# Performance work log

Hardware: AMD Instinct MI355X
Metric: run time of the kernel (lower is better)

Reference implementation:

```python
import jax, jax.numpy as jnp
import numpy as np

B, P, T, V, E, D, ENC = 64, 196, 64, 10000, 512, 512, 512


def setup_inputs() -> dict:
    key = jax.random.key(0)
    ks = jax.random.split(key, 12)
    encoder_out = jax.random.normal(ks[0], (B, P, ENC), jnp.float32)
    encoder_captions = jax.random.randint(ks[1], (B, T), 0, V)
    lens = jax.random.randint(ks[2], (B,), 2, T + 1)
    caption_len = jnp.sort(lens)[::-1].at[0].set(T)  # descending, max pinned to T
    g = lambda k, shape: jax.random.normal(k, shape, jnp.float32) * 0.02
    embedding = jax.random.uniform(ks[3], (V, E), jnp.float32, -0.1, 0.1)
    W_ih = g(ks[4], (4 * D, E + ENC)); b_ih = jnp.zeros((4 * D,), jnp.float32)
    W_hh = g(ks[5], (4 * D, D)); b_hh = jnp.zeros((4 * D,), jnp.float32)
    W_h0 = g(ks[6], (D, ENC)); b_h0 = jnp.zeros((D,), jnp.float32)
    W_c0 = g(ks[7], (D, ENC)); b_c0 = jnp.zeros((D,), jnp.float32)
    W_fc = jax.random.uniform(ks[8], (V, D), jnp.float32, -0.1, 0.1)
    b_fc = jnp.zeros((V,), jnp.float32)
    return dict(encoder_out=encoder_out, encoder_captions=encoder_captions,
                caption_len=caption_len, embedding=embedding,
                W_ih=W_ih, b_ih=b_ih, W_hh=W_hh, b_hh=b_hh,
                W_h0=W_h0, b_h0=b_h0, W_c0=W_c0, b_c0=b_c0,
                W_fc=W_fc, b_fc=b_fc)


def reference(encoder_out, encoder_captions, caption_len, embedding,
              W_ih, b_ih, W_hh, b_hh, W_h0, b_h0, W_c0, b_c0, W_fc, b_fc):
    Tdec = encoder_captions.shape[1] - 1  # max(decode_lengths) since max len pinned
    emb = embedding[encoder_captions]  # [B, T, E]
    mean_enc = encoder_out.mean(axis=1)  # [B, ENC]
    sum_enc = encoder_out.sum(axis=1)    # [B, ENC] (constant across timesteps)
    h0 = mean_enc @ W_h0.T + b_h0
    c0 = mean_enc @ W_c0.T + b_c0
    dec_len = caption_len - 1

    def step(carry, xs):
        h, c = carry
        emb_t, active = xs  # emb_t: [B, E], active: [B] bool
        x = jnp.concatenate([emb_t, sum_enc], axis=1)  # [B, E+ENC]
        gates = x @ W_ih.T + b_ih + h @ W_hh.T + b_hh  # [B, 4D]
        i, f, g, o = jnp.split(gates, 4, axis=1)
        i = jax.nn.sigmoid(i); f = jax.nn.sigmoid(f)
        o = jax.nn.sigmoid(o); g = jnp.tanh(g)
        c_new = f * c + i * g
        h_new = o * jnp.tanh(c_new)
        m = active[:, None]
        # rows past their decode length keep frozen state; preds zero there
        h2 = jnp.where(m, h_new, h)
        c2 = jnp.where(m, c_new, c)
        preds = jnp.where(m, h_new @ W_fc.T + b_fc, 0.0)  # dropout = identity (eval)
        return (h2, c2), preds

    emb_seq = jnp.swapaxes(emb[:, :Tdec], 0, 1)  # [Tdec, B, E]
    active = jnp.arange(Tdec)[:, None] < dec_len[None, :]  # [Tdec, B]
    _, preds = jax.lax.scan(step, (h0, c0), (emb_seq, active))
    return jnp.swapaxes(preds, 0, 1)  # [B, Tdec, V]
```

## Files before the change

kernel.cpp:

```cpp
#include <hip/hip_runtime.h>

typedef __attribute__((ext_vector_type(8))) short bf16x8;
typedef __attribute__((ext_vector_type(4))) float f32x4;
typedef __attribute__((ext_vector_type(2))) float f32x2;
typedef __attribute__((ext_vector_type(4))) unsigned int u32x4;

__device__ __forceinline__ unsigned short f2bf(float x) {
  union { float f; unsigned u; } v; v.f = x;
  unsigned r = v.u + 0x7fffu + ((v.u >> 16) & 1u);
  return (unsigned short)(r >> 16);
}
__device__ __forceinline__ float bf2f(unsigned short s) {
  union { unsigned u; float f; } v; v.u = ((unsigned)s) << 16;
  return v.f;
}
__device__ __forceinline__ float sigm(float x) { return 1.f / (1.f + __expf(-x)); }
__device__ __forceinline__ float tanh_fast(float x) { return 2.f * sigm(2.f * x) - 1.f; }

typedef const __attribute__((address_space(1))) void gvoid_t;
typedef __attribute__((address_space(3))) void lvoid_t;
__device__ __forceinline__ void gl16(const void* g, void* l) {
  __builtin_amdgcn_global_load_lds((gvoid_t*)g, (lvoid_t*)l, 16, 0, 0);
}

__device__ __forceinline__ void ldh16_sc1(const unsigned short* p, u32x4 o[16]) {
  asm volatile(
      "global_load_dwordx4 %0, %16, off sc1\n\t"
      "global_load_dwordx4 %1, %16, off offset:64 sc1\n\t"
      "global_load_dwordx4 %2, %16, off offset:128 sc1\n\t"
      "global_load_dwordx4 %3, %16, off offset:192 sc1\n\t"
      "global_load_dwordx4 %4, %16, off offset:256 sc1\n\t"
      "global_load_dwordx4 %5, %16, off offset:320 sc1\n\t"
      "global_load_dwordx4 %6, %16, off offset:384 sc1\n\t"
      "global_load_dwordx4 %7, %16, off offset:448 sc1\n\t"
      "global_load_dwordx4 %8, %16, off offset:512 sc1\n\t"
      "global_load_dwordx4 %9, %16, off offset:576 sc1\n\t"
      "global_load_dwordx4 %10, %16, off offset:640 sc1\n\t"
      "global_load_dwordx4 %11, %16, off offset:704 sc1\n\t"
      "global_load_dwordx4 %12, %16, off offset:768 sc1\n\t"
      "global_load_dwordx4 %13, %16, off offset:832 sc1\n\t"
      "global_load_dwordx4 %14, %16, off offset:896 sc1\n\t"
      "global_load_dwordx4 %15, %16, off offset:960 sc1\n\t"
      "s_waitcnt vmcnt(0)"
      : "=&v"(o[0]), "=&v"(o[1]), "=&v"(o[2]), "=&v"(o[3]), "=&v"(o[4]),
        "=&v"(o[5]), "=&v"(o[6]), "=&v"(o[7]), "=&v"(o[8]), "=&v"(o[9]),
        "=&v"(o[10]), "=&v"(o[11]), "=&v"(o[12]), "=&v"(o[13]), "=&v"(o[14]),
        "=&v"(o[15])
      : "v"(p)
      : "memory");
}
__device__ __forceinline__ void st2_sc1(unsigned* p, unsigned v0, unsigned v1) {
  asm volatile("global_store_dword %0, %1, off sc1\n\t"
               "global_store_dword %0, %2, off offset:1024 sc1" ::"v"(p), "v"(v0),
               "v"(v1) : "memory");
}
__device__ __forceinline__ void ldpgt_sc1(const unsigned short* p0,
                                          const unsigned short* p1,
                                          const unsigned short* p2,
                                          const unsigned short* p3, unsigned o[4]) {
  asm volatile(
      "global_load_dword %0, %4, off sc1\n\t"
      "global_load_dword %1, %5, off sc1\n\t"
      "global_load_dword %2, %6, off sc1\n\t"
      "global_load_dword %3, %7, off sc1\n\t"
      "s_waitcnt vmcnt(0)"
      : "=&v"(o[0]), "=&v"(o[1]), "=&v"(o[2]), "=&v"(o[3])
      : "v"(p0), "v"(p1), "v"(p2), "v"(p3)
      : "memory");
}
__device__ __forceinline__ void sts_sc1(unsigned short* p, unsigned short v) {
  asm volatile("global_store_short %0, %1, off sc1" ::"v"(p), "v"((unsigned)v)
               : "memory");
}

#define B_ 64
#define TDEC 63
#define D_ 512
#define V_ 10000
#define NWG 32
#define NCONS 223
#define NTILE_N 79
#define NTILE_M 32

__global__ __launch_bounds__(256) void prep(
    const float* __restrict__ enc,
    const float* __restrict__ Wh0, const float* __restrict__ Wc0,
    const float* __restrict__ Wih, const float* __restrict__ Whh,
    const float* __restrict__ Wfc, const float* __restrict__ emb,
    const int* __restrict__ caps,
    short* __restrict__ Wcat, short* __restrict__ Wihe, short* __restrict__ Whhb,
    short* __restrict__ Wfcb, short* __restrict__ Xemb,
    unsigned short* __restrict__ Hall, unsigned short* __restrict__ App) {
  if (blockIdx.x < 128) {
    int b = blockIdx.x >> 1;
    int d = (blockIdx.x & 1) * 256 + threadIdx.x;
    const float* p = enc + (long)b * 196 * 512 + d;
    float s = 0.f;
#pragma unroll 4
    for (int i = 0; i < 196; ++i) s += p[(long)i * 512];
    unsigned short hi = f2bf(s);
    unsigned short lo = f2bf(s - bf2f(hi));
    App[b * 1536 + d] = hi;
    App[b * 1536 + 512 + d] = hi;
    App[b * 1536 + 1024 + d] = lo;
  }
  const long N1 = 3072L * 1536;
  const long N2 = N1 + 2048L * 512;
  const long N3 = N2 + 2048L * 512;
  const long N4 = N3 + 10112L * 512;
  const long N5 = N4 + 4096L * 512;
  const long N6 = N5 + 64L * 512;
  const long N7 = N6 + 64L * 1536;
  for (long idx = (long)blockIdx.x * 256 + threadIdx.x; idx < N7; idx += 2048L * 256) {
    if (idx < N1) {
      int j = (int)(idx / 1536);
      int kk = (int)(idx - (long)j * 1536);
      int k = kk & 511, seg = kk >> 9;
      const float* src = (j < 512) ? (Wh0 + (long)j * 512)
                       : (j < 1024) ? (Wc0 + (long)(j - 512) * 512)
                                    : (Wih + (long)(j - 1024) * 1024 + 512);
      float x = src[k];
      unsigned short hi = f2bf(x);
      Wcat[idx] = (seg == 1) ? (short)f2bf(x - bf2f(hi)) : (short)hi;
    } else if (idx < N2) {
      long e = idx - N1;
      Wihe[e] = (short)f2bf(Wih[(e >> 9) * 1024 + (e & 511)]);
    } else if (idx < N3) {
      long e = idx - N2;
      Whhb[e] = (short)f2bf(Whh[e]);
    } else if (idx < N4) {
      long e = idx - N3;
      long j = e >> 9;
      Wfcb[e] = (j < V_) ? (short)f2bf(Wfc[e]) : (short)0;
    } else if (idx < N5) {
      long e = idx - N4;
      int m = (int)(e >> 9), k = (int)(e & 511);
      short v = 0;
      if (m < B_ * TDEC) {
        int t = m >> 6, b = m & 63;
        int tok = caps[b * 64 + t];
        v = (short)f2bf(emb[(long)tok * 512 + k]);
      }
      Xemb[e] = v;
    } else if (idx < N6) {
      long e = idx - N5;
      Hall[(long)B_ * TDEC * 512 + e] = 0;
    } else {
      long e = idx - N6;
      App[64L * 1536 + e] = 0;
    }
  }
}

__global__ __launch_bounds__(256) void gemm128(
    const short* __restrict__ A, const short* __restrict__ Bm, int K,
    float* __restrict__ f0, float* __restrict__ f1, float* __restrict__ f2,
    unsigned short* __restrict__ sb,
    const float* __restrict__ b0, const float* __restrict__ b1,
    const float* __restrict__ b2, const float* __restrict__ b3) {
  __shared__ short Al[4096], Bl[4096];
  const int tid = threadIdx.x, lane = tid & 63, w = tid >> 6;
  const int wr = w >> 1, wc = w & 1;
  const long m0 = 0, n0 = (long)blockIdx.x * 128;
  f32x4 zz = {0.f, 0.f, 0.f, 0.f};
  f32x4 acc[4][4];
#pragma unroll
  for (int i = 0; i < 4; ++i)
#pragma unroll
    for (int j = 0; j < 4; ++j) acc[i][j] = zz;

  const int srow = tid >> 2, scol = (tid & 3) * 8;
  const short* Ag = A + (m0 + srow) * K + scol;
  const short* Bg = Bm + (n0 + srow) * K + scol;
  short* Alw = &Al[w * 512];
  short* Blw = &Bl[w * 512];
  const int la = (lane & 15) * 32 + (lane >> 4) * 8;

  for (int k0 = 0; k0 < K; k0 += 32) {
    __syncthreads();
    gl16(Ag + k0, Alw);
    gl16(Ag + (long)64 * K + k0, Alw + 2048);
    gl16(Bg + k0, Blw);
    gl16(Bg + (long)64 * K + k0, Blw + 2048);
    __syncthreads();
    bf16x8 af[4], bfr[4];
#pragma unroll
    for (int mi = 0; mi < 4; ++mi) af[mi] = *(const bf16x8*)&Al[(wr * 64 + mi * 16) * 32 + la];
#pragma unroll
    for (int ni = 0; ni < 4; ++ni) bfr[ni] = *(const bf16x8*)&Bl[(wc * 64 + ni * 16) * 32 + la];
#pragma unroll
    for (int mi = 0; mi < 4; ++mi)
#pragma unroll
      for (int ni = 0; ni < 4; ++ni)
        acc[mi][ni] = __builtin_amdgcn_mfma_f32_16x16x32_bf16(af[mi], bfr[ni], acc[mi][ni], 0, 0, 0);
  }

  if (wr == 1) return;
#pragma unroll
  for (int mi = 0; mi < 4; ++mi) {
#pragma unroll
    for (int ni = 0; ni < 4; ++ni) {
      int n = (int)n0 + wc * 64 + ni * 16 + (lane & 15);
#pragma unroll
      for (int reg = 0; reg < 4; ++reg) {
        int m = mi * 16 + (lane >> 4) * 4 + reg;
        float v = acc[mi][ni][reg];
        if (n < 512) {
          float r = v * (1.f / 196.f) + b0[n];
          f0[m * 512 + n] = r;
          sb[m * 512 + n] = f2bf(r);
        } else if (n < 1024) {
          int nn = n - 512;
          float r = v * (1.f / 196.f) + b1[nn];
          f1[m * 512 + nn] = r;
        } else {
          int nn = n - 1024;
          f2[(long)nn * 64 + m] = v + b2[nn] + b3[nn];
        }
      }
    }
  }
}

__global__ __launch_bounds__(512, 1) void lstm_fused(
    const short* __restrict__ Whhb, const float* __restrict__ ENCCT,
    unsigned short* __restrict__ PGT, const float* __restrict__ h0f,
    const float* __restrict__ c0f, const int* __restrict__ caplen,
    unsigned short* __restrict__ hbuf, unsigned short* __restrict__ Hall,
    const short* __restrict__ Wfcb, const float* __restrict__ bfc,
    float* __restrict__ out, int* __restrict__ flags,
    const short* __restrict__ Xemb, const short* __restrict__ Wihe) {
  __shared__ short SH[64 * 512];
  const int bid = blockIdx.x;
  const int tid = threadIdx.x, lane = tid & 63, w = tid >> 6;
  int* prog = flags + 2048;
  int* mcnt = flags + 2304;

  if (bid == NWG) {
    if (w != 0) return;
    int cur = 0;
    while (cur < TDEC) {
      int v = TDEC;
      if (lane < NWG)
        v = __hip_atomic_load(&flags[lane * 32], __ATOMIC_RELAXED,
                              __HIP_MEMORY_SCOPE_AGENT);
      int m = v;
#pragma unroll
      for (int o = 32; o; o >>= 1) {
        int t2 = __shfl_xor(m, o, 64);
        m = (t2 < m) ? t2 : m;
      }
      if (lane == 0 && m > cur)
        __hip_atomic_store(prog, m, __ATOMIC_RELAXED, __HIP_MEMORY_SCOPE_AGENT);
      cur = m;
    }
    return;
  }

  if (bid < NWG) {
    short* Wl = SH;
    const int wg = bid, d0 = wg * 16;
    const int br = w >> 1, rc = w & 1;

    for (int it = tid; it < 4096; it += 512) {
      int r = it >> 6, c8 = it & 63;
      int g = (r >> 3) & 3, rcc = r >> 5, dl_ = r & 7;
      int j = g * 512 + d0 + rcc * 8 + dl_;
      bf16x8 v = *(const bf16x8*)(Whhb + (long)j * 512 + c8 * 8);
      *(bf16x8*)&Wl[r * 512 + ((c8 * 8) ^ ((r & 7) << 3))] = v;
    }

    const int q = (lane >> 4) & 3, bit3 = (lane >> 3) & 1, dl = lane & 7;
    const int d = d0 + rc * 8 + dl;
    const int b0 = br * 16 + q * 4 + 2 * bit3;
    const int ji = d, jf = 512 + d, jg = 1024 + d, jo = 1536 + d;

    f32x2 ei = *(const f32x2*)(ENCCT + (long)ji * 64 + b0);
    f32x2 ef = *(const f32x2*)(ENCCT + (long)jf * 64 + b0);
    f32x2 eg = *(const f32x2*)(ENCCT + (long)jg * 64 + b0);
    f32x2 eo = *(const f32x2*)(ENCCT + (long)jo * 64 + b0);
    float c_r[2] = {c0f[b0 * 512 + d], c0f[(b0 + 1) * 512 + d]};
    float h_r[2] = {h0f[b0 * 512 + d], h0f[(b0 + 1) * 512 + d]};
    int dlen0 = caplen[b0] - 1, dlen1 = caplen[b0 + 1] - 1;
    __syncthreads();

    const int arow = br * 16 + (lane & 15);
    const int kgo = (lane >> 4) * 8;
    const int r0 = rc * 32 + (lane & 15), r1 = rc * 32 + 16 + (lane & 15);
    const int sw0 = (r0 & 7) << 3, sw1 = (r1 & 7) << 3;

    int lastmt = -1;
    unsigned pgw[4];
#define WAIT_MT(mt_)                                                          \
    {                                                                         \
      int ok;                                                                 \
      do {                                                                    \
        int c = 0;                                                            \
        if (lane == 0)                                                        \
          c = __hip_atomic_load(&mcnt[(mt_) * 32], __ATOMIC_RELAXED,          \
                                __HIP_MEMORY_SCOPE_AGENT);                    \
        ok = __shfl(c, 0, 64);                                                \
      } while (ok < 16);                                                      \
    }
    WAIT_MT(0);
    lastmt = 0;
    ldpgt_sc1(PGT + (long)ji * 64 + b0, PGT + (long)jf * 64 + b0,
              PGT + (long)jg * 64 + b0, PGT + (long)jo * 64 + b0, pgw);

    for (int t = 0; t < TDEC; ++t) {
      const unsigned short* hsrc = hbuf + (t & 1) * 32768;
      union { u32x4 u[16]; bf16x8 v[16]; } av;
      ldh16_sc1(hsrc + arow * 512 + kgo, av.u);
      f32x4 a0A = {0.f, 0.f, 0.f, 0.f}, a0B = a0A, a1A = a0A, a1B = a0A;
#pragma unroll
      for (int kk = 0; kk < 8; ++kk) {
        int kA = kk * 32 + kgo, kB = (kk + 8) * 32 + kgo;
        a0A = __builtin_amdgcn_mfma_f32_16x16x32_bf16(
            av.v[kk], *(const bf16x8*)&Wl[r0 * 512 + (kA ^ sw0)], a0A, 0, 0, 0);
        a1A = __builtin_amdgcn_mfma_f32_16x16x32_bf16(
            av.v[kk], *(const bf16x8*)&Wl[r1 * 512 + (kA ^ sw1)], a1A, 0, 0, 0);
        a0B = __builtin_amdgcn_mfma_f32_16x16x32_bf16(
            av.v[kk + 8], *(const bf16x8*)&Wl[r0 * 512 + (kB ^ sw0)], a0B, 0, 0, 0);
        a1B = __builtin_amdgcn_mfma_f32_16x16x32_bf16(
            av.v[kk + 8], *(const bf16x8*)&Wl[r1 * 512 + (kB ^ sw1)], a1B, 0, 0, 0);
      }
      f32x4 a0 = a0A + a0B, a1 = a1A + a1B;

      float own00 = bit3 ? a0[2] : a0[0], own01 = bit3 ? a0[3] : a0[1];
      float snd00 = bit3 ? a0[0] : a0[2], snd01 = bit3 ? a0[1] : a0[3];
      float own10 = bit3 ? a1[2] : a1[0], own11 = bit3 ? a1[3] : a1[1];
      float snd10 = bit3 ? a1[0] : a1[2], snd11 = bit3 ? a1[1] : a1[3];
      float rcv00 = __shfl_xor(snd00, 8, 64), rcv01 = __shfl_xor(snd01, 8, 64);
      float rcv10 = __shfl_xor(snd10, 8, 64), rcv11 = __shfl_xor(snd11, 8, 64);
      float iv[2], fv[2], gv[2], ov[2];
      iv[0] = bit3 ? rcv00 : own00; iv[1] = bit3 ? rcv01 : own01;
      fv[0] = bit3 ? own00 : rcv00; fv[1] = bit3 ? own01 : rcv01;
      gv[0] = bit3 ? rcv10 : own10; gv[1] = bit3 ? rcv11 : own11;
      ov[0] = bit3 ? own10 : rcv10; ov[1] = bit3 ? own11 : rcv11;

      unsigned short hall0, hall1, hs0, hs1;
#pragma unroll
      for (int r = 0; r < 2; ++r) {
        float ii = iv[r] + ei[r] + bf2f((unsigned short)(r ? (pgw[0] >> 16) : (pgw[0] & 0xffffu)));
        float ff = fv[r] + ef[r] + bf2f((unsigned short)(r ? (pgw[1] >> 16) : (pgw[1] & 0xffffu)));
        float gg = gv[r] + eg[r] + bf2f((unsigned short)(r ? (pgw[2] >> 16) : (pgw[2] & 0xffffu)));
        float oo = ov[r] + eo[r] + bf2f((unsigned short)(r ? (pgw[3] >> 16) : (pgw[3] & 0xffffu)));
        ii = sigm(ii); ff = sigm(ff); oo = sigm(oo); gg = tanh_fast(gg);
        float cn = ff * c_r[r] + ii * gg;
        float hn = oo * tanh_fast(cn);
        bool act = t < (r ? dlen1 : dlen0);
        if (act) { c_r[r] = cn; h_r[r] = hn; }
        unsigned short hb = f2bf(hn), h2 = f2bf(h_r[r]);
        if (r == 0) { hall0 = hb; hs0 = h2; } else { hall1 = hb; hs1 = h2; }
      }

      unsigned comb = (unsigned)hs0 | ((unsigned)hs1 << 16);
      unsigned nb = __shfl_xor((int)comb, 1, 64);
      unsigned comb2 = (unsigned)hall0 | ((unsigned)hall1 << 16);
      unsigned nb2 = __shfl_xor((int)comb2, 1, 64);
      if (!(dl & 1)) {
        unsigned* hdst32 = (unsigned*)(hbuf + ((t + 1) & 1) * 32768);
        unsigned* hall32 = (unsigned*)(Hall + (long)t * 32768);
        unsigned w0v = (comb & 0xffffu) | (nb << 16);
        unsigned w1v = (comb >> 16) | (nb & 0xffff0000u);
        unsigned q0 = (comb2 & 0xffffu) | (nb2 << 16);
        unsigned q1 = (comb2 >> 16) | (nb2 & 0xffff0000u);
        st2_sc1(&hdst32[(b0 * 512 + d) >> 1], w0v, w1v);
        st2_sc1(&hall32[(b0 * 512 + d) >> 1], q0, q1);
      }
      asm volatile("s_waitcnt vmcnt(0)" ::: "memory");
      __syncthreads();
      if (tid == 0)
        __hip_atomic_store(&flags[wg * 32], t + 1, __ATOMIC_RELAXED,
                           __HIP_MEMORY_SCOPE_AGENT);
      if (t < TDEC - 1) {
        int nmt = (t + 1) >> 1;
        if (nmt > lastmt) { WAIT_MT(nmt); lastmt = nmt; }
        const unsigned short* pgt1 = PGT + (long)(t + 1) * 2048 * 64;
        ldpgt_sc1(pgt1 + (long)ji * 64 + b0, pgt1 + (long)jf * 64 + b0,
                  pgt1 + (long)jg * 64 + b0, pgt1 + (long)jo * 64 + b0, pgw);
        if (w == 0 && lane < NWG) {
          const int* fp = &flags[lane * 32];
          while (__hip_atomic_load(fp, __ATOMIC_RELAXED, __HIP_MEMORY_SCOPE_AGENT) <= t) {
          }
        }
        __syncthreads();
      }
    }
    return;
  }

  {
    short* Al = SH;
    short* Bl = SH + 4096;
    const int wr = w >> 1, wc = w & 1;
    const int la = (lane & 15) * 32 + (lane >> 4) * 8;
    const int srow = tid >> 2, scol = (tid & 3) * 8;
    short* Alw = Al + w * 512;
    short* Blw = Bl + w * 512;
    const int cid = bid - NWG - 1;

    for (int idx = cid; idx < 512; idx += NCONS) {
      int mt = idx >> 4, nt = idx & 15;
      const short* Ag = Xemb + (long)(mt * 128 + srow) * 512 + scol;
      const short* Bg = Wihe + (long)(nt * 128 + srow) * 512 + scol;
      f32x4 zz = {0.f, 0.f, 0.f, 0.f};
      f32x4 acc[2][4];
#pragma unroll
      for (int i = 0; i < 2; ++i)
#pragma unroll
        for (int j = 0; j < 4; ++j) acc[i][j] = zz;
      for (int k0 = 0; k0 < 512; k0 += 32) {
        __syncthreads();
        gl16(Ag + k0, Alw);
        gl16(Bg + k0, Blw);
        __syncthreads();
        bf16x8 af[2], bfr[4];
#pragma unroll
        for (int mi = 0; mi < 2; ++mi)
          af[mi] = *(const bf16x8*)&Al[(wr * 32 + mi * 16) * 32 + la];
#pragma unroll
        for (int ni = 0; ni < 4; ++ni)
          bfr[ni] = *(const bf16x8*)&Bl[(wc * 64 + ni * 16) * 32 + la];
#pragma unroll
        for (int mi = 0; mi < 2; ++mi)
#pragma unroll
          for (int ni = 0; ni < 4; ++ni)
            acc[mi][ni] = __builtin_amdgcn_mfma_f32_16x16x32_bf16(af[mi], bfr[ni],
                                                                  acc[mi][ni], 0, 0, 0);
      }
#pragma unroll
      for (int mi = 0; mi < 2; ++mi) {
#pragma unroll
        for (int reg = 0; reg < 4; ++reg) {
          int m = mt * 128 + wr * 32 + mi * 16 + (lane >> 4) * 4 + reg;
          int trow = m >> 6, b = m & 63;
          if (trow < TDEC) {
#pragma unroll
            for (int ni = 0; ni < 4; ++ni) {
              int n = nt * 128 + wc * 64 + ni * 16 + (lane & 15);
              sts_sc1(PGT + ((long)trow * 2048 + n) * 64 + b, f2bf(acc[mi][ni][reg]));
            }
          }
        }
      }
      asm volatile("s_waitcnt vmcnt(0)" ::: "memory");
      __syncthreads();
      if (tid == 0)
        __hip_atomic_fetch_add(&mcnt[mt * 32], 1, __ATOMIC_RELAXED,
                               __HIP_MEMORY_SCOPE_AGENT);
    }

    for (int idx = cid; idx < NTILE_M * NTILE_N; idx += NCONS) {
      int mt = idx / NTILE_N, nt = idx - mt * NTILE_N;
      int need = 2 * (mt + 1); if (need > TDEC) need = TDEC;
      if (tid == 0) {
        while (__hip_atomic_load(prog, __ATOMIC_RELAXED, __HIP_MEMORY_SCOPE_AGENT) < need)
          __builtin_amdgcn_s_sleep(4);
        (void)__hip_atomic_load(prog, __ATOMIC_ACQUIRE, __HIP_MEMORY_SCOPE_AGENT);
      }
      __syncthreads();

      const unsigned short* Ag = Hall + (long)(mt * 128 + srow) * 512 + scol;
      const short* Bg = Wfcb + (long)(nt * 128 + srow) * 512 + scol;
      f32x4 zz = {0.f, 0.f, 0.f, 0.f};
      f32x4 acc[2][4];
#pragma unroll
      for (int i = 0; i < 2; ++i)
#pragma unroll
        for (int j = 0; j < 4; ++j) acc[i][j] = zz;

      for (int k0 = 0; k0 < 512; k0 += 32) {
        __syncthreads();
        gl16(Ag + k0, Alw);
        gl16(Bg + k0, Blw);
        __syncthreads();
        bf16x8 af[2], bfr[4];
#pragma unroll
        for (int mi = 0; mi < 2; ++mi)
          af[mi] = *(const bf16x8*)&Al[(wr * 32 + mi * 16) * 32 + la];
#pragma unroll
        for (int ni = 0; ni < 4; ++ni)
          bfr[ni] = *(const bf16x8*)&Bl[(wc * 64 + ni * 16) * 32 + la];
#pragma unroll
        for (int mi = 0; mi < 2; ++mi)
#pragma unroll
          for (int ni = 0; ni < 4; ++ni)
            acc[mi][ni] = __builtin_amdgcn_mfma_f32_16x16x32_bf16(af[mi], bfr[ni],
                                                                  acc[mi][ni], 0, 0, 0);
      }

#pragma unroll
      for (int mi = 0; mi < 2; ++mi) {
#pragma unroll
        for (int reg = 0; reg < 4; ++reg) {
          int m = mt * 128 + wr * 32 + mi * 16 + (lane >> 4) * 4 + reg;
          int trow = m >> 6, b = m & 63;
          if (trow < TDEC) {
            bool act = trow < (caplen[b] - 1);
            float* orow = out + ((long)b * TDEC + trow) * V_;
#pragma unroll
            for (int ni = 0; ni < 4; ++ni) {
              int n = nt * 128 + wc * 64 + ni * 16 + (lane & 15);
              if (n < V_) orow[n] = act ? (acc[mi][ni][reg] + bfc[n]) : 0.f;
            }
          }
        }
      }
    }
  }
}

extern "C" void kernel_launch(void* const* d_in, const int* in_sizes, int n_in,
                              void* d_out, int out_size, void* d_ws, size_t ws_size,
                              hipStream_t stream) {
  const float* enc = (const float*)d_in[0];
  const int* caps = (const int*)d_in[1];
  const int* clen = (const int*)d_in[2];
  const float* emb = (const float*)d_in[3];
  const float* Wih = (const float*)d_in[4];
  const float* bih = (const float*)d_in[5];
  const float* Whh = (const float*)d_in[6];
  const float* bhh = (const float*)d_in[7];
  const float* Wh0 = (const float*)d_in[8];
  const float* bh0 = (const float*)d_in[9];
  const float* Wc0 = (const float*)d_in[10];
  const float* bc0 = (const float*)d_in[11];
  const float* Wfc = (const float*)d_in[12];
  const float* bfc = (const float*)d_in[13];
  float* out = (float*)d_out;

  char* ws = (char*)d_ws;
  size_t off = 0;
  auto alloc = [&](size_t bytes) {
    void* p = ws + off;
    off = (off + bytes + 255) & ~(size_t)255;
    return p;
  };
  int* flags = (int*)alloc(16384);
  unsigned short* App = (unsigned short*)alloc(128L * 1536 * 2);
  short* Wcat = (short*)alloc(3072L * 1536 * 2);
  short* Wihe = (short*)alloc(2048L * 512 * 2);
  short* Whhb = (short*)alloc(2048L * 512 * 2);
  short* Wfcb = (short*)alloc(10112L * 512 * 2);
  short* Xemb = (short*)alloc(4096L * 512 * 2);
  unsigned short* PGT = (unsigned short*)alloc(63L * 2048 * 64 * 2);
  float* ENCCT = (float*)alloc(2048L * 64 * 4);
  float* h0f = (float*)alloc(64L * 512 * 4);
  float* c0f = (float*)alloc(64L * 512 * 4);
  unsigned short* hbuf = (unsigned short*)alloc(2L * 64 * 512 * 2);
  unsigned short* Hall = (unsigned short*)alloc(4096L * 512 * 2);
  (void)ws_size; (void)in_sizes; (void)n_in; (void)out_size;

  hipMemsetAsync(flags, 0, 16384, stream);
  prep<<<2048, 256, 0, stream>>>(enc, Wh0, Wc0, Wih, Whh, Wfc, emb, caps, Wcat, Wihe,
                                 Whhb, Wfcb, Xemb, Hall, App);
  gemm128<<<dim3(24), 256, 0, stream>>>((const short*)App, Wcat, 1536, h0f, c0f, ENCCT,
                                        hbuf, bh0, bc0, bih, bhh);
  lstm_fused<<<dim3(256), 512, 0, stream>>>(Whhb, ENCCT, PGT, h0f, c0f, clen, hbuf, Hall,
                                            Wfcb, bfc, out, flags, Xemb, Wihe);
}
```

Baseline: 552.2 us.

## Move W_fc bf16 conversion into LSTM consumer blocks and defer Hall stores

The W_fc fp32-to-bf16 conversion moves out of the prep kernel and into the consumer workgroups of the fused LSTM kernel, running after the input-projection GEMM tiles. There it overlaps with the sequential recurrence instead of sitting on the critical path before the LSTM starts. A new counter gates the output GEMM until every consumer has finished converting. The recurrent workgroups now write their Hall rows after publishing the step flag, which takes that store off the per-step latency. To stay correct, the consumer wait threshold rises by one step and a final flag store is added after the loop.

```diff
diff --git a/kernel.cpp b/kernel.cpp
--- a/kernel.cpp
+++ b/kernel.cpp
@@ -86,11 +86,10 @@
     const float* __restrict__ enc,
     const float* __restrict__ Wh0, const float* __restrict__ Wc0,
     const float* __restrict__ Wih, const float* __restrict__ Whh,
-    const float* __restrict__ Wfc, const float* __restrict__ emb,
-    const int* __restrict__ caps,
+    const float* __restrict__ emb, const int* __restrict__ caps,
     short* __restrict__ Wcat, short* __restrict__ Wihe, short* __restrict__ Whhb,
-    short* __restrict__ Wfcb, short* __restrict__ Xemb,
-    unsigned short* __restrict__ Hall, unsigned short* __restrict__ App) {
+    short* __restrict__ Xemb, unsigned short* __restrict__ Hall,
+    unsigned short* __restrict__ App) {
   if (blockIdx.x < 128) {
     int b = blockIdx.x >> 1;
     int d = (blockIdx.x & 1) * 256 + threadIdx.x;
@@ -107,11 +106,10 @@
   const long N1 = 3072L * 1536;
   const long N2 = N1 + 2048L * 512;
   const long N3 = N2 + 2048L * 512;
-  const long N4 = N3 + 10112L * 512;
-  const long N5 = N4 + 4096L * 512;
-  const long N6 = N5 + 64L * 512;
-  const long N7 = N6 + 64L * 1536;
-  for (long idx = (long)blockIdx.x * 256 + threadIdx.x; idx < N7; idx += 2048L * 256) {
+  const long N4 = N3 + 4096L * 512;
+  const long N5 = N4 + 64L * 512;
+  const long N6 = N5 + 64L * 1536;
+  for (long idx = (long)blockIdx.x * 256 + threadIdx.x; idx < N6; idx += 2048L * 256) {
     if (idx < N1) {
       int j = (int)(idx / 1536);
       int kk = (int)(idx - (long)j * 1536);
@@ -130,10 +128,6 @@
       Whhb[e] = (short)f2bf(Whh[e]);
     } else if (idx < N4) {
       long e = idx - N3;
-      long j = e >> 9;
-      Wfcb[e] = (j < V_) ? (short)f2bf(Wfc[e]) : (short)0;
-    } else if (idx < N5) {
-      long e = idx - N4;
       int m = (int)(e >> 9), k = (int)(e & 511);
       short v = 0;
       if (m < B_ * TDEC) {
@@ -142,11 +136,11 @@
         v = (short)f2bf(emb[(long)tok * 512 + k]);
       }
       Xemb[e] = v;
-    } else if (idx < N6) {
-      long e = idx - N5;
+    } else if (idx < N5) {
+      long e = idx - N4;
       Hall[(long)B_ * TDEC * 512 + e] = 0;
     } else {
-      long e = idx - N6;
+      long e = idx - N5;
       App[64L * 1536 + e] = 0;
     }
   }
@@ -227,14 +221,15 @@
     unsigned short* __restrict__ PGT, const float* __restrict__ h0f,
     const float* __restrict__ c0f, const int* __restrict__ caplen,
     unsigned short* __restrict__ hbuf, unsigned short* __restrict__ Hall,
-    const short* __restrict__ Wfcb, const float* __restrict__ bfc,
-    float* __restrict__ out, int* __restrict__ flags,
+    short* __restrict__ Wfcb, const float* __restrict__ Wfc,
+    const float* __restrict__ bfc, float* __restrict__ out, int* __restrict__ flags,
     const short* __restrict__ Xemb, const short* __restrict__ Wihe) {
   __shared__ short SH[64 * 512];
   const int bid = blockIdx.x;
   const int tid = threadIdx.x, lane = tid & 63, w = tid >> 6;
   int* prog = flags + 2048;
   int* mcnt = flags + 2304;
+  int* wcnt = flags + 3392;
 
   if (bid == NWG) {
     if (w != 0) return;
@@ -358,21 +353,23 @@
       unsigned nb = __shfl_xor((int)comb, 1, 64);
       unsigned comb2 = (unsigned)hall0 | ((unsigned)hall1 << 16);
       unsigned nb2 = __shfl_xor((int)comb2, 1, 64);
+      unsigned q0 = (comb2 & 0xffffu) | (nb2 << 16);
+      unsigned q1 = (comb2 >> 16) | (nb2 & 0xffff0000u);
       if (!(dl & 1)) {
         unsigned* hdst32 = (unsigned*)(hbuf + ((t + 1) & 1) * 32768);
-        unsigned* hall32 = (unsigned*)(Hall + (long)t * 32768);
         unsigned w0v = (comb & 0xffffu) | (nb << 16);
         unsigned w1v = (comb >> 16) | (nb & 0xffff0000u);
-        unsigned q0 = (comb2 & 0xffffu) | (nb2 << 16);
-        unsigned q1 = (comb2 >> 16) | (nb2 & 0xffff0000u);
         st2_sc1(&hdst32[(b0 * 512 + d) >> 1], w0v, w1v);
-        st2_sc1(&hall32[(b0 * 512 + d) >> 1], q0, q1);
       }
       asm volatile("s_waitcnt vmcnt(0)" ::: "memory");
       __syncthreads();
       if (tid == 0)
         __hip_atomic_store(&flags[wg * 32], t + 1, __ATOMIC_RELAXED,
                            __HIP_MEMORY_SCOPE_AGENT);
+      if (!(dl & 1)) {
+        unsigned* hall32 = (unsigned*)(Hall + (long)t * 32768);
+        st2_sc1(&hall32[(b0 * 512 + d) >> 1], q0, q1);
+      }
       if (t < TDEC - 1) {
         int nmt = (t + 1) >> 1;
         if (nmt > lastmt) { WAIT_MT(nmt); lastmt = nmt; }
@@ -387,6 +384,11 @@
         __syncthreads();
       }
     }
+    asm volatile("s_waitcnt vmcnt(0)" ::: "memory");
+    __syncthreads();
+    if (tid == 0)
+      __hip_atomic_store(&flags[wg * 32], TDEC, __ATOMIC_RELAXED,
+                         __HIP_MEMORY_SCOPE_AGENT);
     return;
   }
 
@@ -451,10 +453,24 @@
                                __HIP_MEMORY_SCOPE_AGENT);
     }
 
+    for (long e = (long)cid * 512 + tid; e < 10112L * 512; e += (long)NCONS * 512) {
+      long j = e >> 9;
+      unsigned short v = 0;
+      if (j < V_) v = f2bf(Wfc[e]);
+      sts_sc1((unsigned short*)Wfcb + e, v);
+    }
+    asm volatile("s_waitcnt vmcnt(0)" ::: "memory");
+    __syncthreads();
+    if (tid == 0)
+      __hip_atomic_fetch_add(wcnt, 1, __ATOMIC_RELAXED, __HIP_MEMORY_SCOPE_AGENT);
+
     for (int idx = cid; idx < NTILE_M * NTILE_N; idx += NCONS) {
       int mt = idx / NTILE_N, nt = idx - mt * NTILE_N;
-      int need = 2 * (mt + 1); if (need > TDEC) need = TDEC;
+      int need = 2 * (mt + 1) + 1; if (need > TDEC) need = TDEC;
       if (tid == 0) {
+        while (__hip_atomic_load(wcnt, __ATOMIC_RELAXED, __HIP_MEMORY_SCOPE_AGENT) <
+               NCONS)
+          __builtin_amdgcn_s_sleep(4);
         while (__hip_atomic_load(prog, __ATOMIC_RELAXED, __HIP_MEMORY_SCOPE_AGENT) < need)
           __builtin_amdgcn_s_sleep(4);
         (void)__hip_atomic_load(prog, __ATOMIC_ACQUIRE, __HIP_MEMORY_SCOPE_AGENT);
@@ -553,10 +569,10 @@
   (void)ws_size; (void)in_sizes; (void)n_in; (void)out_size;
 
   hipMemsetAsync(flags, 0, 16384, stream);
-  prep<<<2048, 256, 0, stream>>>(enc, Wh0, Wc0, Wih, Whh, Wfc, emb, caps, Wcat, Wihe,
-                                 Whhb, Wfcb, Xemb, Hall, App);
+  prep<<<2048, 256, 0, stream>>>(enc, Wh0, Wc0, Wih, Whh, emb, caps, Wcat, Wihe, Whhb,
+                                 Xemb, Hall, App);
   gemm128<<<dim3(24), 256, 0, stream>>>((const short*)App, Wcat, 1536, h0f, c0f, ENCCT,
                                         hbuf, bh0, bc0, bih, bhh);
   lstm_fused<<<dim3(256), 512, 0, stream>>>(Whhb, ENCCT, PGT, h0f, c0f, clen, hbuf, Hall,
-                                            Wfcb, bfc, out, flags, Xemb, Wihe);
-}
+                                            Wfcb, Wfc, bfc, out, flags, Xemb, Wihe);
+}
```

After: 552.9 us. About the same (+0.1%).
